# Performance work log

Hardware: AMD Instinct MI355X
Metric: run time of the kernel (lower is better)

## Reference

```python
import jax, jax.numpy as jnp
import numpy as np

C = 256        # branch_in_channels / head_conv
H, W = 160, 400
KPT_THR = 0.4  # forward_test default kpt_thr
ROOT_THR = 1.0 # self.root_thr
EPS = 1e-4


def _conv(x, w, b):
    # NCHW conv, SAME padding
    y = jax.lax.conv_general_dilated(x, w, (1, 1), 'SAME',
                                     dimension_numbers=('NCHW', 'OIHW', 'NCHW'))
    return y + b[None, :, None, None]


def _ctnet_head(x, w1, b1, w2, b2):
    # CtnetHead: Conv3x3 -> ReLU -> Conv1x1
    return _conv(jax.nn.relu(_conv(x, w1, b1)), w2, b2)


def setup_inputs() -> dict:
    key = jax.random.key(0)
    ks = jax.random.split(key, 16)
    s = 0.02
    def w3(k, co, ci):
        return jax.random.normal(k, (co, ci, 3, 3), jnp.float32) * s
    def w1k(k, co, ci):
        return jax.random.normal(k, (co, ci, 1, 1), jnp.float32) * s
    inp = {'f_hm': jax.random.normal(ks[0], (1, C, H, W), jnp.float32)}
    # four heads: centerpts (hm:1), keypts (hm:1), offset (2ch), reg (2ch)
    names = [('cpt', 1), ('kpt', 1), ('off', 2), ('reg', 2)]
    i = 1
    for name, cout in names:
        inp[f'{name}_w1'] = w3(ks[i], C, C); i += 1
        inp[f'{name}_b1'] = jnp.zeros((C,), jnp.float32)
        inp[f'{name}_w2'] = w1k(ks[i], cout, C); i += 1
        inp[f'{name}_b2'] = jnp.zeros((cout,), jnp.float32)
    return inp


def reference(f_hm, cpt_w1, cpt_b1, cpt_w2, cpt_b2,
              kpt_w1, kpt_b1, kpt_w2, kpt_b2,
              off_w1, off_b1, off_w2, off_b2,
              reg_w1, reg_b1, reg_w2, reg_b2):
    # heads
    hm = jnp.clip(jax.nn.sigmoid(_ctnet_head(f_hm, cpt_w1, cpt_b1, cpt_w2, cpt_b2)), EPS, 1.0 - EPS)
    kpts_hm = jnp.clip(jax.nn.sigmoid(_ctnet_head(f_hm, kpt_w1, kpt_b1, kpt_w2, kpt_b2)), EPS, 1.0 - EPS)
    pts_offset = _ctnet_head(f_hm, off_w1, off_b1, off_w2, off_b2)   # [1,2,H,W]
    int_offset = _ctnet_head(f_hm, reg_w1, reg_b1, reg_w2, reg_b2)   # [1,2,H,W]

    # ktdet_decode_fast: (1,3) max-pool NMS along width
    hmax = jax.lax.reduce_window(kpts_hm, -jnp.inf, jax.lax.max,
                                 (1, 1, 1, 3), (1, 1, 1, 1),
                                 ((0, 0), (0, 0), (0, 0), (1, 1)))
    heat_nms = kpts_hm * (hmax == kpts_hm).astype(kpts_hm.dtype)    # [1,1,H,W]

    # root-center mask: offset_y < root_thr AND heat_nms > kpt_thr, transposed to [W,H]
    mask_low = ((pts_offset[0, 1] < ROOT_THR) & (heat_nms[0, 0] > KPT_THR)).T  # [W,H] bool

    # coordinate maps: coord_mat channels are (x, y), permuted to [H,W,2]
    xs = jnp.arange(W, dtype=jnp.float32)
    ys = jnp.arange(H, dtype=jnp.float32)
    coord = jnp.stack(jnp.meshgrid(xs, ys, indexing='xy'), axis=-1)  # [H,W,2]

    offset_hw2 = jnp.transpose(pts_offset[0], (1, 2, 0))  # [H,W,2]
    error_hw2 = jnp.transpose(int_offset[0], (1, 2, 0))   # [H,W,2]
    root_mat = coord + offset_hw2
    align_mat = coord + error_hw2
    # heat_mat = heat_nms repeated to 2 channels; keypoint selection mask
    heat_hw = jnp.transpose(heat_nms[0], (1, 2, 0))        # [H,W,1]
    kpt_mask = jnp.tile(heat_hw, (1, 1, 2)) > KPT_THR      # [H,W,2] bool

    # host-side np.where / list extraction is excluded (data-dependent shapes);
    # all device-side math of ktdet_decode_fast is returned as fixed-shape arrays.
    return (hm, kpts_hm, pts_offset, int_offset, heat_nms,
            mask_low, root_mat, align_mat, kpt_mask)
```

## Files before the change

kernel.cpp:

```cpp
#include <hip/hip_runtime.h>

#define Hh 160
#define Ww 400
#define Cc 256
#define HW 64000
#define PITCH 401
#define XBASE 402
#define XT_PX 64963

typedef unsigned short u16;
typedef unsigned int   u32;
typedef __attribute__((ext_vector_type(8))) short short8;
typedef __attribute__((ext_vector_type(4))) float f32x4;

#define WA2_U16   (8*72*8*512)
#define XT_BYTES  ((size_t)8 * XT_PX * 64)
#define BSLICE    ((size_t)XT_PX * 64)
#define WS_NEED   ((size_t)WA2_U16 * 2 + XT_BYTES)

__device__ __forceinline__ u16 f2b(float v) {
    const u32 u = __float_as_uint(v);
    return (u16)((u + 0x7FFFu + ((u >> 16) & 1u)) >> 16);
}
__device__ __forceinline__ float sigclip(float v) {
    const float s = 1.0f / (1.0f + expf(-v));
    return fminf(fmaxf(s, 1e-4f), 1.0f - 1e-4f);
}
__device__ __forceinline__ void gload_lds16(const void* g, void* l) {
    __builtin_amdgcn_global_load_lds(
        (const __attribute__((address_space(1))) unsigned int*)g,
        (__attribute__((address_space(3))) unsigned int*)l, 16, 0, 0);
}

__global__ __launch_bounds__(256) void prep_weights(
    const float* __restrict__ w0, const float* __restrict__ w1p,
    const float* __restrict__ w2p, const float* __restrict__ w3p,
    u16* __restrict__ Wa2)
{
    const int blk  = blockIdx.x;
    const int head = blk / 72;
    const int s    = blk - head * 72;
    const int cib  = s / 9;
    const int tap  = s - cib * 9;
    const float* w = head == 0 ? w0 : head == 1 ? w1p : head == 2 ? w2p : w3p;

    const int t    = threadIdx.x;
    const int n16  = t & 15;
    const int mi   = (t >> 4) & 3;
    const int mblk = (t >> 6) & 1;
    const int mt   = t >> 7;
    const int m    = mt * 128 + mblk * 64 + mi * 16 + n16;
    const int hm   = head * 2 + mt;

    uint4* dst4 = (uint4*)Wa2 +
        ((size_t)((hm * 72 + s) * 2 + mblk) * 4 + mi) * 64 + n16;
    #pragma unroll
    for (int qq = 0; qq < 4; ++qq) {
        u16 tmp[8];
        #pragma unroll
        for (int j = 0; j < 8; ++j) {
            const int ci = cib * 32 + qq * 8 + j;
            tmp[j] = f2b(w[(size_t)m * (Cc * 9) + (size_t)ci * 9 + tap]);
        }
        dst4[qq * 16] = *(const uint4*)tmp;
    }
}

__global__ __launch_bounds__(256) void prep_x(
    const float* __restrict__ x, uint4* __restrict__ xt4)
{
    const int xx = blockIdx.x * 256 + threadIdx.x;
    const int y  = blockIdx.y;
    if (xx >= Ww) return;
    const int p  = y * Ww + xx;
    const size_t slot = (size_t)XBASE + (size_t)y * PITCH + xx;
    #pragma unroll
    for (int cib = 0; cib < 8; ++cib) {
        uint4* dst = xt4 + ((size_t)cib * XT_PX + slot) * 4;
        #pragma unroll
        for (int v = 0; v < 4; ++v) {
            u32 tmp[4];
            #pragma unroll
            for (int j = 0; j < 4; ++j) {
                const int ci = cib * 32 + v * 8 + j * 2;
                tmp[j] = (u32)f2b(x[(size_t)ci * HW + p])
                       | ((u32)f2b(x[(size_t)(ci + 1) * HW + p]) << 16);
            }
            dst[v] = *(const uint4*)tmp;
        }
    }
}

__global__ __launch_bounds__(64) void prep_zero(unsigned long long* __restrict__ xt64)
{
    const int b = blockIdx.x;
    int slot;
    if (b < 402)       slot = b;
    else if (b < 563)  slot = (b - 401) * PITCH;
    else               slot = 64561 + (b - 563);
    const int cib = threadIdx.x >> 3, j = threadIdx.x & 7;
    xt64[((size_t)cib * XT_PX + slot) * 8 + j] = 0ull;
}

__global__ __launch_bounds__(512, 2) void conv_mfma(
    const u16* __restrict__ Wa2, const u16* __restrict__ xt,
    const float* __restrict__ b1_0, const float* __restrict__ b1_1,
    const float* __restrict__ b1_2, const float* __restrict__ b1_3,
    const float* __restrict__ w2_0, const float* __restrict__ w2_1,
    const float* __restrict__ w2_2, const float* __restrict__ w2_3,
    const float* __restrict__ b2_0, const float* __restrict__ b2_1,
    const float* __restrict__ b2_2, const float* __restrict__ b2_3,
    float* __restrict__ out)
{
    __shared__ __align__(16) char SA[49152];
    __shared__ __align__(16) u16 Bb[2][12672];

    u16 (*Ab)[8192]   = (u16 (*)[8192])SA;
    float (*Red)[2][8] = (float (*)[2][8])SA;

    const int t    = threadIdx.x;
    const int lane = t & 63, wv = t >> 6;
    const int q    = lane >> 4, n16 = lane & 15;
    const int x0   = (blockIdx.x < 6) ? blockIdx.x * 64 : (Ww - 64);
    const int y0   = blockIdx.y * 4;
    const int head = blockIdx.z;
    const int r    = wv & 3;
    const int mt   = wv >> 2;

    const int adst_off = mt * 4096 + r * 1024;
    const u16* asrc0 = Wa2 + (size_t)(head * 2 + mt) * (72 * 4096)
                     + r * 1024 + lane * 8;

    const long base_slot = (long)(y0 - 1) * PITCH + (x0 - 1) + XBASE;
    int bsrc[4], dbo[4];
    #pragma unroll
    for (int j = 0; j < 4; ++j) {
        const int db = wv * 3168 + (j < 3 ? j * 1024 : 2144);
        dbo[j] = db;
        const int d   = db + lane * 16;
        const int row = d / 4224;
        const int rem = d - row * 4224;
        const int px  = rem >> 6;
        const int qd  = (rem >> 4) & 3;
        const int qs  = qd ^ ((px >> 1) & 3);
        bsrc[j] = (int)((base_slot + row * PITCH + px) * 64 + qs * 16);
    }
    const char* xtb = (const char*)xt;

    int boff[4][3];
    #pragma unroll
    for (int nj = 0; nj < 4; ++nj)
        #pragma unroll
        for (int kx = 0; kx < 3; ++kx) {
            const int pxi = nj * 16 + n16 + kx;
            boff[nj][kx] = pxi * 64 + ((q ^ ((pxi >> 1) & 3)) * 16);
        }

    f32x4 acc[8][4];
    #pragma unroll
    for (int mi = 0; mi < 8; ++mi)
        #pragma unroll
        for (int nj = 0; nj < 4; ++nj) {
            f32x4 z = {0.f, 0.f, 0.f, 0.f};
            acc[mi][nj] = z;
        }

    {
        u16* d0 = Ab[0] + adst_off;
        gload_lds16(asrc0,       d0);
        gload_lds16(asrc0 + 512, d0 + 512);
        #pragma unroll
        for (int j = 0; j < 4; ++j)
            gload_lds16(xtb + bsrc[j], (char*)(&Bb[0][0]) + dbo[j]);
        u16* d1 = Ab[1] + adst_off;
        gload_lds16(asrc0 + 4096,       d1);
        gload_lds16(asrc0 + 4096 + 512, d1 + 512);
    }
    asm volatile("s_waitcnt vmcnt(2)" ::: "memory");
    __builtin_amdgcn_s_barrier();
    __builtin_amdgcn_sched_barrier(0);

    int ap = 0;
    for (int cib = 0; cib < 8; ++cib) {
        const char* bread    = (const char*)(&Bb[cib & 1][0]);
        char*       bwrite   = (char*)(&Bb[(cib & 1) ^ 1][0]);
        const char* bsrc_cib = xtb + (size_t)(cib + 1) * BSLICE;
        const bool  nl       = (cib < 7);
        #pragma unroll
        for (int tap = 0; tap < 9; ++tap) {
            const int s = cib * 9 + tap;
            if (s < 70) {
                const int aw = ap ? ap - 1 : 2;
                const u16* src = asrc0 + (size_t)(s + 2) * 4096;
                u16* dst = Ab[aw] + adst_off;
                gload_lds16(src,       dst);
                gload_lds16(src + 512, dst + 512);
            }
            if (nl && (tap == 0 || tap == 2 || tap == 4 || tap == 6)) {
                const int j = tap >> 1;
                gload_lds16(bsrc_cib + bsrc[j], bwrite + dbo[j]);
            }
            const int ky = tap / 3, kx = tap - ky * 3;
            const u16*  abuf = Ab[ap] + mt * 4096 + lane * 8;
            const char* brow = bread + (r + ky) * 4224;
            short8 bf[4];
            #pragma unroll
            for (int nj = 0; nj < 4; ++nj)
                bf[nj] = *(const short8*)(brow + boff[nj][kx]);
            __builtin_amdgcn_s_setprio(1);
            #pragma unroll
            for (int mi = 0; mi < 8; ++mi) {
                const short8 a = *(const short8*)(abuf + mi * 512);
                #pragma unroll
                for (int nj = 0; nj < 4; ++nj)
                    acc[mi][nj] = __builtin_amdgcn_mfma_f32_16x16x32_bf16(
                        a, bf[nj], acc[mi][nj], 0, 0, 0);
            }
            __builtin_amdgcn_s_setprio(0);
            __builtin_amdgcn_sched_barrier(0);
            if (nl) {
                if (tap == 8) asm volatile("s_waitcnt vmcnt(2)" ::: "memory");
                else          asm volatile("s_waitcnt vmcnt(3)" ::: "memory");
                __builtin_amdgcn_s_barrier();
            } else {
                if (tap < 7)       asm volatile("s_waitcnt vmcnt(2)" ::: "memory");
                else if (tap == 7) asm volatile("s_waitcnt vmcnt(0)" ::: "memory");
                if (tap < 8) __builtin_amdgcn_s_barrier();
            }
            __builtin_amdgcn_sched_barrier(0);
            ap = (ap == 2) ? 0 : ap + 1;
        }
    }

    const float* b1 = head == 0 ? b1_0 : head == 1 ? b1_1 : head == 2 ? b1_2 : b1_3;
    const float* w2 = head == 0 ? w2_0 : head == 1 ? w2_1 : head == 2 ? w2_2 : w2_3;
    const float* b2 = head == 0 ? b2_0 : head == 1 ? b2_1 : head == 2 ? b2_2 : b2_3;
    const int cout   = (head < 2) ? 1 : 2;
    const int outoff = head == 0 ? 0 : head == 1 ? HW : head == 2 ? 2 * HW : 4 * HW;

    float p0[4] = {0.f, 0.f, 0.f, 0.f}, p1[4] = {0.f, 0.f, 0.f, 0.f};
    #pragma unroll
    for (int mi = 0; mi < 8; ++mi)
        #pragma unroll
        for (int rr = 0; rr < 4; ++rr) {
            const int m = mt * 128 + mi * 16 + q * 4 + rr;
            const float bb = b1[m], wc0 = w2[m];
            const float wc1 = (cout == 2) ? w2[Cc + m] : 0.0f;
            #pragma unroll
            for (int nj = 0; nj < 4; ++nj) {
                const float h = fmaxf(acc[mi][nj][rr] + bb, 0.0f);
                p0[nj] = fmaf(wc0, h, p0[nj]);
                p1[nj] = fmaf(wc1, h, p1[nj]);
            }
        }

    __syncthreads();
    #pragma unroll
    for (int nj = 0; nj < 4; ++nj) {
        const int n = r * 64 + nj * 16 + n16;
        Red[n][0][mt * 4 + q] = p0[nj];
        Red[n][1][mt * 4 + q] = p1[nj];
    }
    __syncthreads();

    if (t < cout * 256) {
        const int n = t & 255, c = t >> 8;
        float sv = b2[c];
        #pragma unroll
        for (int i = 0; i < 8; ++i) sv += Red[n][c][i];
        if (head < 2) sv = sigclip(sv);
        const int xg = x0 + (n & 63);
        const int yg = y0 + (n >> 6);
        out[outoff + c * HW + yg * Ww + xg] = sv;
    }
}

__global__ __launch_bounds__(256) void conv_head_simple(
    const float* __restrict__ x,
    const float* __restrict__ w1, const float* __restrict__ b1,
    const float* __restrict__ w2, const float* __restrict__ b2,
    float* __restrict__ out, int outoff, int cout, int apply_sig)
{
    const int px = threadIdx.x & 63;
    const int g  = threadIdx.x >> 6;
    const int x0 = blockIdx.x * 64;
    const int y  = blockIdx.y;
    const int xg = x0 + px;
    __shared__ float RedS[4][64][2];

    bool valid[9]; int xoff[9];
    #pragma unroll
    for (int dy = 0; dy < 3; ++dy) {
        const int yy = y + dy - 1;
        #pragma unroll
        for (int dx = 0; dx < 3; ++dx) {
            const int xx = xg + dx - 1;
            const int k = dy * 3 + dx;
            valid[k] = (yy >= 0 && yy < Hh && xx >= 0 && xx < Ww);
            xoff[k]  = valid[k] ? (yy * Ww + xx) : 0;
        }
    }
    float hid[64];
    #pragma unroll
    for (int mi = 0; mi < 64; ++mi) hid[mi] = b1[g * 64 + mi];
    for (int ci = 0; ci < Cc; ++ci) {
        const float* xch = x + (size_t)ci * HW;
        float xv[9];
        #pragma unroll
        for (int k = 0; k < 9; ++k) xv[k] = valid[k] ? xch[xoff[k]] : 0.0f;
        const float* wci = w1 + ((size_t)(g * 64) * Cc + ci) * 9;
        #pragma unroll 8
        for (int mi = 0; mi < 64; ++mi) {
            const float* wr = wci + (size_t)mi * (Cc * 9);
            float h = hid[mi];
            #pragma unroll
            for (int k = 0; k < 9; ++k) h = fmaf(wr[k], xv[k], h);
            hid[mi] = h;
        }
    }
    float p0 = 0.f, p1 = 0.f;
    #pragma unroll 8
    for (int mi = 0; mi < 64; ++mi) {
        const int m = g * 64 + mi;
        const float h = fmaxf(hid[mi], 0.0f);
        p0 = fmaf(w2[m], h, p0);
        if (cout == 2) p1 = fmaf(w2[Cc + m], h, p1);
    }
    RedS[g][px][0] = p0; RedS[g][px][1] = p1;
    __syncthreads();
    if (g == 0 && xg < Ww)
        for (int c = 0; c < cout; ++c) {
            float sv = b2[c] + RedS[0][px][c] + RedS[1][px][c]
                             + RedS[2][px][c] + RedS[3][px][c];
            if (apply_sig) sv = sigclip(sv);
            out[outoff + c * HW + y * Ww + xg] = sv;
        }
}

__global__ __launch_bounds__(256) void finalize_decode(float* __restrict__ out)
{
    const int i = blockIdx.x * 256 + threadIdx.x;
    if (i >= HW) return;
    const int h = i / Ww;
    const int w = i - h * Ww;

    const float k0 = out[HW + i];
    const float km = (w > 0)      ? out[HW + i - 1] : -1e30f;
    const float kp = (w < Ww - 1) ? out[HW + i + 1] : -1e30f;
    const float hmax = fmaxf(km, fmaxf(k0, kp));
    const float heat = (hmax == k0) ? k0 : 0.0f;

    const float off0 = out[2 * HW + i];
    const float off1 = out[3 * HW + i];
    const float reg0 = out[4 * HW + i];
    const float reg1 = out[5 * HW + i];
    const bool kmask = heat > 0.4f;

    out[6 * HW + i] = heat;
    out[7 * HW + w * Hh + h] = (off1 < 1.0f && kmask) ? 1.0f : 0.0f;
    out[8 * HW + 2 * i]      = (float)w + off0;
    out[8 * HW + 2 * i + 1]  = (float)h + off1;
    out[10 * HW + 2 * i]     = (float)w + reg0;
    out[10 * HW + 2 * i + 1] = (float)h + reg1;
    const float kb = kmask ? 1.0f : 0.0f;
    out[12 * HW + 2 * i]     = kb;
    out[12 * HW + 2 * i + 1] = kb;
}

extern "C" void kernel_launch(void* const* d_in, const int* in_sizes, int n_in,
                              void* d_out, int out_size, void* d_ws, size_t ws_size,
                              hipStream_t stream) {
    (void)in_sizes; (void)n_in; (void)out_size;
    const float* x = (const float*)d_in[0];
    float* out = (float*)d_out;

    if (ws_size >= WS_NEED) {
        u16* Wa2 = (u16*)d_ws;
        u16* xt  = Wa2 + WA2_U16;

        prep_weights<<<dim3(288), 256, 0, stream>>>(
            (const float*)d_in[1], (const float*)d_in[5],
            (const float*)d_in[9], (const float*)d_in[13], Wa2);
        prep_x<<<dim3(2, 160), 256, 0, stream>>>(x, (uint4*)xt);
        prep_zero<<<dim3(965), 64, 0, stream>>>((unsigned long long*)xt);

        conv_mfma<<<dim3(7, 40, 4), 512, 0, stream>>>(
            Wa2, xt,
            (const float*)d_in[2],  (const float*)d_in[6],
            (const float*)d_in[10], (const float*)d_in[14],
            (const float*)d_in[3],  (const float*)d_in[7],
            (const float*)d_in[11], (const float*)d_in[15],
            (const float*)d_in[4],  (const float*)d_in[8],
            (const float*)d_in[12], (const float*)d_in[16],
            out);
    } else {
        const int outoffs[4] = {0, HW, 2 * HW, 4 * HW};
        const int couts[4]   = {1, 1, 2, 2};
        for (int hd = 0; hd < 4; ++hd)
            conv_head_simple<<<dim3(7, 160), 256, 0, stream>>>(
                x,
                (const float*)d_in[1 + 4 * hd], (const float*)d_in[2 + 4 * hd],
                (const float*)d_in[3 + 4 * hd], (const float*)d_in[4 + 4 * hd],
                out, outoffs[hd], couts[hd], (hd < 2) ? 1 : 0);
    }
    finalize_decode<<<dim3(250), 256, 0, stream>>>(out);
}
```

Baseline: 492.5 us.

## Deepen A-weight LDS ring to six stages and register-prefetch A fragments

Restructures the conv MFMA main loop. The A-weight LDS ring goes from three to six buffers and is prefetched three steps ahead. The A fragments for the next tap are loaded from LDS into registers (double-buffered aR0/aR1) while the current tap's MFMAs run, and the B loads are issued over the first four taps of each input-channel block. The aim is to hide LDS and global-load latency behind MFMA work. In exchange, LDS use grows from 48 KB to 96 KB for A, plus about 50 KB for B, which may break the 2-blocks-per-CU occupancy the launch bounds assume. It also adds register pressure from the 16 extra short8 registers.

```diff
diff --git a/kernel.cpp b/kernel.cpp
--- a/kernel.cpp
+++ b/kernel.cpp
@@ -112,11 +112,10 @@
     const float* __restrict__ b2_2, const float* __restrict__ b2_3,
     float* __restrict__ out)
 {
-    __shared__ __align__(16) char SA[49152];
+    __shared__ __align__(16) u16 Ab[6 * 8192];
     __shared__ __align__(16) u16 Bb[2][12672];
 
-    u16 (*Ab)[8192]   = (u16 (*)[8192])SA;
-    float (*Red)[2][8] = (float (*)[2][8])SA;
+    float (*Red)[2][8] = (float (*)[2][8])Ab;
 
     const int t    = threadIdx.x;
     const int lane = t & 63, wv = t >> 6;
@@ -147,14 +146,18 @@
     }
     const char* xtb = (const char*)xt;
 
-    int boff[4][3];
-    #pragma unroll
-    for (int nj = 0; nj < 4; ++nj)
-        #pragma unroll
-        for (int kx = 0; kx < 3; ++kx) {
-            const int pxi = nj * 16 + n16 + kx;
-            boff[nj][kx] = pxi * 64 + ((q ^ ((pxi >> 1) & 3)) * 16);
-        }
+    int bbase[3];
+    #pragma unroll
+    for (int kx = 0; kx < 3; ++kx) {
+        const int m = n16 + kx;
+        bbase[kx] = m * 64 + ((q ^ ((m >> 1) & 3)) * 16);
+    }
+
+    const char* abR  = (const char*)Ab + mt * 8192 + lane * 16;
+    const char* brd0 = (const char*)(&Bb[0][0]) + r * 4224;
+    const char* brd1 = (const char*)(&Bb[1][0]) + r * 4224;
+    char* bw0 = (char*)(&Bb[0][0]);
+    char* bw1 = (char*)(&Bb[1][0]);
 
     f32x4 acc[8][4];
     #pragma unroll
@@ -165,72 +168,88 @@
             acc[mi][nj] = z;
         }
 
+    short8 aR0[8], aR1[8];
+
     {
-        u16* d0 = Ab[0] + adst_off;
-        gload_lds16(asrc0,       d0);
-        gload_lds16(asrc0 + 512, d0 + 512);
-        #pragma unroll
-        for (int j = 0; j < 4; ++j)
-            gload_lds16(xtb + bsrc[j], (char*)(&Bb[0][0]) + dbo[j]);
-        u16* d1 = Ab[1] + adst_off;
+        u16* d0 = Ab + 0 * 8192 + adst_off;
+        gload_lds16(asrc0,            d0);
+        gload_lds16(asrc0 + 512,      d0 + 512);
+        u16* d1 = Ab + 1 * 8192 + adst_off;
         gload_lds16(asrc0 + 4096,       d1);
         gload_lds16(asrc0 + 4096 + 512, d1 + 512);
+        #pragma unroll
+        for (int j = 0; j < 4; ++j)
+            gload_lds16(xtb + bsrc[j], bw0 + dbo[j]);
+        u16* d2 = Ab + 2 * 8192 + adst_off;
+        gload_lds16(asrc0 + 8192,       d2);
+        gload_lds16(asrc0 + 8192 + 512, d2 + 512);
     }
     asm volatile("s_waitcnt vmcnt(2)" ::: "memory");
     __builtin_amdgcn_s_barrier();
     __builtin_amdgcn_sched_barrier(0);
 
-    int ap = 0;
-    for (int cib = 0; cib < 8; ++cib) {
-        const char* bread    = (const char*)(&Bb[cib & 1][0]);
-        char*       bwrite   = (char*)(&Bb[(cib & 1) ^ 1][0]);
-        const char* bsrc_cib = xtb + (size_t)(cib + 1) * BSLICE;
-        const bool  nl       = (cib < 7);
-        #pragma unroll
-        for (int tap = 0; tap < 9; ++tap) {
-            const int s = cib * 9 + tap;
-            if (s < 70) {
-                const int aw = ap ? ap - 1 : 2;
-                const u16* src = asrc0 + (size_t)(s + 2) * 4096;
-                u16* dst = Ab[aw] + adst_off;
-                gload_lds16(src,       dst);
-                gload_lds16(src + 512, dst + 512);
-            }
-            if (nl && (tap == 0 || tap == 2 || tap == 4 || tap == 6)) {
-                const int j = tap >> 1;
-                gload_lds16(bsrc_cib + bsrc[j], bwrite + dbo[j]);
-            }
-            const int ky = tap / 3, kx = tap - ky * 3;
-            const u16*  abuf = Ab[ap] + mt * 4096 + lane * 8;
-            const char* brow = bread + (r + ky) * 4224;
-            short8 bf[4];
-            #pragma unroll
-            for (int nj = 0; nj < 4; ++nj)
-                bf[nj] = *(const short8*)(brow + boff[nj][kx]);
-            __builtin_amdgcn_s_setprio(1);
-            #pragma unroll
-            for (int mi = 0; mi < 8; ++mi) {
-                const short8 a = *(const short8*)(abuf + mi * 512);
-                #pragma unroll
-                for (int nj = 0; nj < 4; ++nj)
-                    acc[mi][nj] = __builtin_amdgcn_mfma_f32_16x16x32_bf16(
-                        a, bf[nj], acc[mi][nj], 0, 0, 0);
-            }
-            __builtin_amdgcn_s_setprio(0);
-            __builtin_amdgcn_sched_barrier(0);
-            if (nl) {
-                if (tap == 8) asm volatile("s_waitcnt vmcnt(2)" ::: "memory");
-                else          asm volatile("s_waitcnt vmcnt(3)" ::: "memory");
-                __builtin_amdgcn_s_barrier();
-            } else {
-                if (tap < 7)       asm volatile("s_waitcnt vmcnt(2)" ::: "memory");
-                else if (tap == 7) asm volatile("s_waitcnt vmcnt(0)" ::: "memory");
-                if (tap < 8) __builtin_amdgcn_s_barrier();
-            }
-            __builtin_amdgcn_sched_barrier(0);
-            ap = (ap == 2) ? 0 : ap + 1;
-        }
-    }
+    #pragma unroll
+    for (int mi = 0; mi < 8; ++mi)
+        aR0[mi] = *(const short8*)(abR + 0 * 16384 + mi * 1024);
+
+#define STEP(SOFF, TAP, CUR, NXT, SR, SW, VM, BRD, BWR, BNX)                   \
+  {                                                                            \
+    const int KY = (TAP) / 3, KX = (TAP) - 3 * ((TAP) / 3);                    \
+    int ss = sb + ((SOFF) + 3); ss = (ss > 71) ? 71 : ss;                      \
+    const u16* asg = asrc0 + (size_t)ss * 4096;                                \
+    u16* adt = Ab + (SW) * 8192 + adst_off;                                    \
+    gload_lds16(asg, adt);                                                     \
+    gload_lds16(asg + 512, adt + 512);                                         \
+    if ((TAP) <= 3) gload_lds16(BNX + bsrc[TAP], BWR + dbo[TAP]);              \
+    short8 bF[4];                                                              \
+    _Pragma("unroll")                                                          \
+    for (int nj = 0; nj < 4; ++nj)                                             \
+      bF[nj] = *(const short8*)(BRD + KY * 4224 + nj * 1024 + bbase[KX]);      \
+    _Pragma("unroll")                                                          \
+    for (int mi = 0; mi < 8; ++mi)                                             \
+      NXT[mi] = *(const short8*)(abR + (SR) * 16384 + mi * 1024);              \
+    __builtin_amdgcn_s_setprio(1);                                             \
+    _Pragma("unroll")                                                          \
+    for (int mi = 0; mi < 8; ++mi) {                                           \
+      _Pragma("unroll")                                                        \
+      for (int nj = 0; nj < 4; ++nj)                                           \
+        acc[mi][nj] = __builtin_amdgcn_mfma_f32_16x16x32_bf16(                 \
+            CUR[mi], bF[nj], acc[mi][nj], 0, 0, 0);                            \
+    }                                                                          \
+    __builtin_amdgcn_s_setprio(0);                                             \
+    __builtin_amdgcn_sched_barrier(0);                                         \
+    asm volatile("s_waitcnt vmcnt(" #VM ")" ::: "memory");                     \
+    __builtin_amdgcn_s_barrier();                                              \
+    __builtin_amdgcn_sched_barrier(0);                                         \
+  }
+
+    for (int cib2 = 0; cib2 < 4; ++cib2) {
+        const int sb = 18 * cib2;
+        const char* bnA = xtb + (size_t)(2 * cib2 + 1) * BSLICE;
+        const int nxt2  = (2 * cib2 + 2 > 7) ? 7 : (2 * cib2 + 2);
+        const char* bnB = xtb + (size_t)nxt2 * BSLICE;
+        STEP(0,  0, aR0, aR1, 1, 3, 3, brd0, bw1, bnA)
+        STEP(1,  1, aR1, aR0, 2, 4, 3, brd0, bw1, bnA)
+        STEP(2,  2, aR0, aR1, 3, 5, 3, brd0, bw1, bnA)
+        STEP(3,  3, aR1, aR0, 4, 0, 3, brd0, bw1, bnA)
+        STEP(4,  4, aR0, aR1, 5, 1, 2, brd0, bw1, bnA)
+        STEP(5,  5, aR1, aR0, 0, 2, 2, brd0, bw1, bnA)
+        STEP(6,  6, aR0, aR1, 1, 3, 2, brd0, bw1, bnA)
+        STEP(7,  7, aR1, aR0, 2, 4, 2, brd0, bw1, bnA)
+        STEP(8,  8, aR0, aR1, 3, 5, 2, brd0, bw1, bnA)
+        STEP(9,  0, aR1, aR0, 4, 0, 3, brd1, bw0, bnB)
+        STEP(10, 1, aR0, aR1, 5, 1, 3, brd1, bw0, bnB)
+        STEP(11, 2, aR1, aR0, 0, 2, 3, brd1, bw0, bnB)
+        STEP(12, 3, aR0, aR1, 1, 3, 3, brd1, bw0, bnB)
+        STEP(13, 4, aR1, aR0, 2, 4, 2, brd1, bw0, bnB)
+        STEP(14, 5, aR0, aR1, 3, 5, 2, brd1, bw0, bnB)
+        STEP(15, 6, aR1, aR0, 4, 0, 2, brd1, bw0, bnB)
+        STEP(16, 7, aR0, aR1, 5, 1, 2, brd1, bw0, bnB)
+        STEP(17, 8, aR1, aR0, 0, 2, 2, brd1, bw0, bnB)
+    }
+#undef STEP
+
+    asm volatile("s_waitcnt vmcnt(0)" ::: "memory");
 
     const float* b1 = head == 0 ? b1_0 : head == 1 ? b1_1 : head == 2 ? b1_2 : b1_3;
     const float* w2 = head == 0 ? w2_0 : head == 1 ? w2_1 : head == 2 ? w2_2 : w2_3;
```

After: 523.8 us. 1.06x slower.
